# Kernel tuning notes

Hardware: AMD Instinct MI355X
Metric: run time of the kernel (lower is better)

The kernel has to match this reference:

```python
import jax, jax.numpy as jnp
import numpy as np

N_NODES = 20000
N_EDGES = 320000
N_GRAPHS = 256
F_IN = 128
HID = 512


def _xavier(key, shape, gain=1.0):
    fan_out, fan_in = shape
    a = gain * np.sqrt(6.0 / (fan_in + fan_out))
    return jax.random.uniform(key, shape, jnp.float32, -a, a)


def setup_inputs() -> dict:
    key = jax.random.key(0)
    ks = jax.random.split(key, 9)
    x = jax.random.normal(ks[0], (N_NODES, F_IN), jnp.float32)
    edge_index = jax.random.randint(ks[1], (2, N_EDGES), 0, N_NODES, dtype=jnp.int64)
    batch = jnp.sort(jax.random.randint(ks[2], (N_NODES,), 0, N_GRAPHS, dtype=jnp.int64))
    return {
        "x": x,
        "edge_index": edge_index,
        "batch": batch,
        "lin_W": _xavier(ks[3], (HID, F_IN)),
        "lin_b": jnp.zeros((HID,), jnp.float32),
        "W1": _xavier(ks[4], (HID, F_IN)),
        "b1": jnp.zeros((HID,), jnp.float32),
        "W2": _xavier(ks[5], (HID, HID)),
        "b2": jnp.zeros((HID,), jnp.float32),
        "W3": _xavier(ks[6], (HID, HID)),
        "b3": jnp.zeros((HID,), jnp.float32),
        "W4": _xavier(ks[7], (HID, HID)),
        "b4": jnp.zeros((HID,), jnp.float32),
    }


def _gcn_conv(x, W, b, src, dst, norm, n_nodes):
    # PyG GCNConv: h = x @ W.T; out_i = sum_j norm_ij * h_j (scatter over dst) + b
    h = x @ W.T
    msg = h[src] * norm[:, None]  # [E', H] gather + scale
    return jax.ops.segment_sum(msg, dst, num_segments=n_nodes) + b


def reference(x, edge_index, batch, lin_W, lin_b, W1, b1, W2, b2, W3, b3, W4, b4):
    n = x.shape[0]
    loop = jnp.arange(n, dtype=edge_index.dtype)
    src = jnp.concatenate([edge_index[0], loop])
    dst = jnp.concatenate([edge_index[1], loop])
    # symmetric normalization D^-1/2 (A+I) D^-1/2, degree = in-degree over dst
    deg = jax.ops.segment_sum(jnp.ones_like(src, dtype=x.dtype), dst, num_segments=n)
    dis = jnp.where(deg > 0, jax.lax.rsqrt(deg), 0.0)
    norm = dis[src] * dis[dst]

    x_l = x @ lin_W.T + lin_b  # dead code when act=None (kept for faithfulness)

    h1 = _gcn_conv(x, W1, b1, src, dst, norm, n)
    h2 = _gcn_conv(h1, W2, b2, src, dst, norm, n)
    h3 = _gcn_conv(h2, W3, b3, src, dst, norm, n)
    h4 = _gcn_conv(h3, W4, b4, src, dst, norm, n)
    h = jnp.concatenate([h1, h2, h3, h4], axis=1)  # [N, 4*HID]

    h_pooled = jax.ops.segment_max(h, batch, num_segments=N_GRAPHS)
    h_pos = (h > 0).astype(h.dtype)
    counts = jax.ops.segment_sum(jnp.ones((n,), h.dtype), batch, num_segments=N_GRAPHS)
    h_pos_pooled = jax.ops.segment_sum(h_pos, batch, num_segments=N_GRAPHS) / jnp.maximum(counts, 1.0)[:, None]
    return jnp.concatenate([h_pooled, h_pos_pooled], axis=1)  # [G, 8*HID]
```

## Files before the change

kernel.cpp:

```cpp
#include <hip/hip_runtime.h>
#include <cfloat>
#include <cmath>

#define F_IN 128
#define HID 512

typedef short bf16x8 __attribute__((ext_vector_type(8)));
typedef float f32x4 __attribute__((ext_vector_type(4)));
typedef short s16x4 __attribute__((ext_vector_type(4)));

__device__ static inline void split_bf16(float v, short& hi, short& lo) {
    unsigned u = __float_as_uint(v);
    unsigned r = u + 0x7FFF + ((u >> 16) & 1);
    hi = (short)(r >> 16);
    float hf = __uint_as_float(((unsigned)(unsigned short)hi) << 16);
    float res = v - hf;
    unsigned u2 = __float_as_uint(res);
    unsigned r2 = u2 + 0x7FFF + ((u2 >> 16) & 1);
    lo = (short)(r2 >> 16);
}

__device__ static inline void gload_lds16(const void* g, void* l) {
    __builtin_amdgcn_global_load_lds(
        (const __attribute__((address_space(1))) unsigned int*)g,
        (__attribute__((address_space(3))) unsigned int*)l,
        16, 0, 0);
}


__global__ void zero_kernel(int* __restrict__ a, int n) {
    int i = blockIdx.x * blockDim.x + threadIdx.x;
    if (i < n) a[i] = 0;
}

__global__ void count_in_kernel(const int* __restrict__ dst, int* __restrict__ cnt, int E) {
    int e = blockIdx.x * blockDim.x + threadIdx.x;
    if (e < E) atomicAdd(&cnt[dst[e]], 1);
}

__global__ void scan_kernel(const int* __restrict__ cnt, int* __restrict__ offs, int n) {
    __shared__ int buf[1024];
    __shared__ int carry_s;
    if (threadIdx.x == 0) carry_s = 0;
    __syncthreads();
    for (int base = 0; base < n; base += 1024) {
        int i = base + threadIdx.x;
        int v = (i < n) ? cnt[i] : 0;
        buf[threadIdx.x] = v;
        __syncthreads();
        for (int s = 1; s < 1024; s <<= 1) {
            int t = (threadIdx.x >= s) ? buf[threadIdx.x - s] : 0;
            __syncthreads();
            buf[threadIdx.x] += t;
            __syncthreads();
        }
        int total = buf[1023];
        if (i < n) offs[i] = carry_s + buf[threadIdx.x] - v;
        __syncthreads();
        if (threadIdx.x == 0) carry_s += total;
        __syncthreads();
    }
    if (threadIdx.x == 0) offs[n] = carry_s;
}

__global__ void dis_starts_kernel(const int* __restrict__ offs, float* __restrict__ dis,
                                  float* __restrict__ rdis,
                                  const int* __restrict__ batch, int* __restrict__ starts,
                                  int n, int G) {
    int i = blockIdx.x * blockDim.x + threadIdx.x;
    if (i >= n) return;
    float degp1 = (float)(offs[i + 1] - offs[i] + 1);
    dis[i] = rsqrtf(degp1);
    rdis[i] = sqrtf(degp1);
    int b = batch[i];
    if (i == 0) {
        for (int g = 0; g <= b; g++) starts[g] = 0;
    } else {
        int bp = batch[i - 1];
        for (int g = bp + 1; g <= b; g++) starts[g] = i;
    }
    if (i == n - 1) {
        for (int g = b + 1; g <= G; g++) starts[g] = n;
    }
}

__global__ void fill_csr_kernel(const int* __restrict__ src, const int* __restrict__ dst,
                                const int* __restrict__ offs, int* __restrict__ cnt,
                                unsigned short* __restrict__ csr, int E) {
    int e = blockIdx.x * blockDim.x + threadIdx.x;
    if (e < E) {
        int d = dst[e];
        int p = atomicSub(&cnt[d], 1);
        csr[offs[d] + p - 1] = (unsigned short)src[e];
    }
}

__global__ void wconv_kernel(const float* __restrict__ W1, const float* __restrict__ W2,
                             const float* __restrict__ W3, const float* __restrict__ W4,
                             short* __restrict__ Whi, short* __restrict__ Wlo) {
    int i = blockIdx.x * blockDim.x + threadIdx.x;
    const int n1 = HID * F_IN, nk = HID * HID;
    float v;
    if (i < n1) v = W1[i];
    else if (i < n1 + nk) v = W2[i - n1];
    else if (i < n1 + 2 * nk) v = W3[i - n1 - nk];
    else if (i < n1 + 3 * nk) v = W4[i - n1 - 2 * nk];
    else return;
    short h, l;
    split_bf16(v, h, l);
    Whi[i] = h;
    Wlo[i] = l;
}

__global__ void xscale_kernel(const float* __restrict__ x, const float* __restrict__ dis,
                              float* __restrict__ xs, int total) {
    int i = blockIdx.x * blockDim.x + threadIdx.x;
    if (i < total) xs[i] = x[i] * dis[i >> 7];
}

template <int F, int CHUNKS>
__global__ __launch_bounds__(256) void agg_gather4_kernel(
    const float* __restrict__ Hs, const float* __restrict__ dis,
    const int* __restrict__ offs, const unsigned short* __restrict__ csr,
    short* __restrict__ Ahi, short* __restrict__ Alo, int n) {
    constexpr int CW = 128;
    int blk = blockIdx.x;
    int chunk = blk & (CHUNKS - 1);
    int gt = blk / CHUNKS;
    int wave = threadIdx.x >> 6;
    int i = gt * 4 + wave;
    if (i >= n) return;

    int tid = threadIdx.x & 63;
    int es = tid >> 5;
    int lq = tid & 31;
    int colbase = chunk * CW + lq * 4;
    const float* Hbase = Hs + colbase;

    int e0 = offs[i], e1 = offs[i + 1];
    float di = dis[i];

    f32x4 acc = (f32x4){0.f, 0.f, 0.f, 0.f};
    if (es == 0) acc = *(const f32x4*)(Hbase + (size_t)i * F);

    for (int w0 = e0; w0 < e1; w0 += 64) {
        int cnt = e1 - w0; if (cnt > 64) cnt = 64;
        int idx = n;
        if (tid < cnt) idx = csr[w0 + tid];
        int nb4 = (cnt + 7) >> 3;
        for (int b = 0; b < nb4; b++) {
            int base = b * 8 + es;
            int j0 = __shfl(idx, base,     64);
            int j1 = __shfl(idx, base + 2, 64);
            int j2 = __shfl(idx, base + 4, 64);
            int j3 = __shfl(idx, base + 6, 64);
            f32x4 r0 = *(const f32x4*)(Hbase + (size_t)j0 * F);
            f32x4 r1 = *(const f32x4*)(Hbase + (size_t)j1 * F);
            f32x4 r2 = *(const f32x4*)(Hbase + (size_t)j2 * F);
            f32x4 r3 = *(const f32x4*)(Hbase + (size_t)j3 * F);
            acc[0] += (r0[0] + r1[0]) + (r2[0] + r3[0]);
            acc[1] += (r0[1] + r1[1]) + (r2[1] + r3[1]);
            acc[2] += (r0[2] + r1[2]) + (r2[2] + r3[2]);
            acc[3] += (r0[3] + r1[3]) + (r2[3] + r3[3]);
        }
    }
    acc[0] += __shfl_xor(acc[0], 32, 64);
    acc[1] += __shfl_xor(acc[1], 32, 64);
    acc[2] += __shfl_xor(acc[2], 32, 64);
    acc[3] += __shfl_xor(acc[3], 32, 64);

    if (es == 0) {
        short h[4], l[4];
        #pragma unroll
        for (int q = 0; q < 4; q++) split_bf16(acc[q] * di, h[q], l[q]);
        *(s16x4*)&Ahi[(size_t)i * F + colbase] = (s16x4){h[0], h[1], h[2], h[3]};
        *(s16x4*)&Alo[(size_t)i * F + colbase] = (s16x4){l[0], l[1], l[2], l[3]};
    }
}

__global__ __launch_bounds__(256) void gemm_mfma_kernel(
    const short* __restrict__ Ahi, const short* __restrict__ Alo,
    const short* __restrict__ Whi, const short* __restrict__ Wlo,
    const float* __restrict__ bias, const float* __restrict__ dis,
    float* __restrict__ Hs,
    int M, int K, int Nout, int MT, int MT8) {
    __shared__ __attribute__((aligned(16))) short lds[12288];

    int blk = blockIdx.x;
    int xcd = blk & 7;
    int r = blk >> 3;
    int n0t = r & 7;
    int mt = xcd * MT8 + (r >> 3);
    if (mt >= MT) return;
    int m0 = mt * 128, n0 = n0t * 64;

    int tid = threadIdx.x;
    int w = tid >> 6, l = tid & 63;
    int lrow = l & 15, lq = l >> 4;
    int w6 = w * 6;

    f32x4 acc[4][2];
    #pragma unroll
    for (int i = 0; i < 4; i++)
        #pragma unroll
        for (int j = 0; j < 2; j++) acc[i][j] = (f32x4){0.f, 0.f, 0.f, 0.f};

    int wm = w >> 1, wn = w & 1;

    for (int k0 = 0; k0 < K; k0 += 32) {
        #pragma unroll
        for (int t = 0; t < 6; t++) {
            int s = w6 + t;
            const short* pl;
            int prow;
            if (s < 8)       { pl = Ahi; prow = m0 + 16 * s; }
            else if (s < 16) { pl = Alo; prow = m0 + 16 * (s - 8); }
            else if (s < 20) { pl = Whi; prow = n0 + 16 * (s - 16); }
            else             { pl = Wlo; prow = n0 + 16 * (s - 20); }
            gload_lds16(pl + (size_t)(prow + lrow) * K + (k0 + lq * 8), &lds[s * 512]);
        }
        __syncthreads();

        bf16x8 ah[4], al[4], wh[2], wl[2];
        #pragma unroll
        for (int i = 0; i < 4; i++) {
            ah[i] = *(const bf16x8*)&lds[((wm * 4 + i) * 64 + l) * 8];
            al[i] = *(const bf16x8*)&lds[((8 + wm * 4 + i) * 64 + l) * 8];
        }
        #pragma unroll
        for (int j = 0; j < 2; j++) {
            wh[j] = *(const bf16x8*)&lds[((16 + wn * 2 + j) * 64 + l) * 8];
            wl[j] = *(const bf16x8*)&lds[((20 + wn * 2 + j) * 64 + l) * 8];
        }
        #pragma unroll
        for (int i = 0; i < 4; i++)
            #pragma unroll
            for (int j = 0; j < 2; j++) {
                acc[i][j] = __builtin_amdgcn_mfma_f32_16x16x32_bf16(ah[i], wh[j], acc[i][j], 0, 0, 0);
                acc[i][j] = __builtin_amdgcn_mfma_f32_16x16x32_bf16(ah[i], wl[j], acc[i][j], 0, 0, 0);
                acc[i][j] = __builtin_amdgcn_mfma_f32_16x16x32_bf16(al[i], wh[j], acc[i][j], 0, 0, 0);
            }
        __syncthreads();
    }

    float dv[4][4];
    #pragma unroll
    for (int i = 0; i < 4; i++) {
        int mrow = m0 + (wm * 4 + i) * 16 + lq * 4;
        #pragma unroll
        for (int rr = 0; rr < 4; rr++) {
            int mm = mrow + rr;
            dv[i][rr] = (mm < M) ? dis[mm] : 0.0f;
        }
    }

    #pragma unroll
    for (int j = 0; j < 2; j++) {
        int col = n0 + (wn * 2 + j) * 16 + lrow;
        float bv = bias[col];
        #pragma unroll
        for (int i = 0; i < 4; i++) {
            int mrow = m0 + (wm * 4 + i) * 16 + lq * 4;
            #pragma unroll
            for (int rr = 0; rr < 4; rr++) {
                int mm = mrow + rr;
                if (mm < M) Hs[(size_t)mm * Nout + col] = dv[i][rr] * (acc[i][j][rr] + bv);
            }
        }
    }
}

__global__ __launch_bounds__(64) void pool_kernel(
    const float* __restrict__ Hs, const float* __restrict__ rdis,
    const int* __restrict__ starts,
    float* __restrict__ out, int layer) {
    int g = blockIdx.x;
    int c = blockIdx.y * 64 + threadIdx.x;
    int s = starts[g], e = starts[g + 1];
    float mx = -INFINITY;
    int pos = 0;
    #pragma unroll 4
    for (int n = s; n < e; n++) {
        float v = Hs[(size_t)n * HID + c] * rdis[n];
        mx = fmaxf(mx, v);
        pos += (v > 0.0f) ? 1 : 0;
    }
    float cntf = fmaxf((float)(e - s), 1.0f);
    out[(size_t)g * (8 * HID) + layer * HID + c] = mx;
    out[(size_t)g * (8 * HID) + 4 * HID + layer * HID + c] = (float)pos / cntf;
}

extern "C" void kernel_launch(void* const* d_in, const int* in_sizes, int n_in,
                              void* d_out, int out_size, void* d_ws, size_t ws_size,
                              hipStream_t stream) {
    const float* x     = (const float*)d_in[0];
    const int*   eidx  = (const int*)d_in[1];
    const int*   batch = (const int*)d_in[2];
    const float* W1 = (const float*)d_in[5];
    const float* b1 = (const float*)d_in[6];
    const float* W2 = (const float*)d_in[7];
    const float* b2 = (const float*)d_in[8];
    const float* W3 = (const float*)d_in[9];
    const float* b3 = (const float*)d_in[10];
    const float* W4 = (const float*)d_in[11];
    const float* b4 = (const float*)d_in[12];
    float* out = (float*)d_out;

    const int N = in_sizes[0] / F_IN;
    const int E = in_sizes[1] / 2;
    const int G = out_size / (8 * HID);

    const int* src = eidx;
    const int* dst = eidx + E;

    const size_t nW = (size_t)HID * F_IN + 3 * (size_t)HID * HID;
    char* w = (char*)d_ws;
    short* Ahi = (short*)w; w += (size_t)N * HID * sizeof(short);
    short* Alo = (short*)w; w += (size_t)N * HID * sizeof(short);
    float* Hs  = (float*)w; w += (size_t)(N + 1) * HID * sizeof(float);
    float* xs  = (float*)w; w += (size_t)(N + 1) * F_IN * sizeof(float);
    short* Whi = (short*)w; w += nW * sizeof(short);
    short* Wlo = (short*)w; w += nW * sizeof(short);
    int* offs  = (int*)w;   w += (size_t)(N + 4) * sizeof(int);
    unsigned short* csr = (unsigned short*)w; w += (size_t)E * sizeof(unsigned short);
    int* cnt   = (int*)w;   w += (size_t)N * sizeof(int);
    float* dis = (float*)w; w += (size_t)N * sizeof(float);
    float* rdis = (float*)w; w += (size_t)N * sizeof(float);
    int* starts = (int*)w;  w += (size_t)(G + 1) * sizeof(int);

    const size_t wo1 = 0;
    const size_t wo2 = (size_t)HID * F_IN;
    const size_t wo3 = wo2 + (size_t)HID * HID;
    const size_t wo4 = wo3 + (size_t)HID * HID;

    const int TB = 256;
    zero_kernel<<<(N + TB - 1) / TB, TB, 0, stream>>>(cnt, N);
    zero_kernel<<<(HID + TB - 1) / TB, TB, 0, stream>>>((int*)(Hs + (size_t)N * HID), HID);
    zero_kernel<<<1, TB, 0, stream>>>((int*)(xs + (size_t)N * F_IN), F_IN);
    count_in_kernel<<<(E + TB - 1) / TB, TB, 0, stream>>>(dst, cnt, E);
    scan_kernel<<<1, 1024, 0, stream>>>(cnt, offs, N);
    dis_starts_kernel<<<(N + TB - 1) / TB, TB, 0, stream>>>(offs, dis, rdis, batch, starts, N, G);
    fill_csr_kernel<<<(E + TB - 1) / TB, TB, 0, stream>>>(src, dst, offs, cnt, csr, E);
    wconv_kernel<<<((int)nW + TB - 1) / TB, TB, 0, stream>>>(W1, W2, W3, W4, Whi, Wlo);
    xscale_kernel<<<(N * F_IN + TB - 1) / TB, TB, 0, stream>>>(x, dis, xs, N * F_IN);

    const int MT = (N + 127) / 128;
    const int MT8 = (MT + 7) / 8;
    const int gemm_blocks = 8 * MT8 * 8;
    dim3 pool_grid(G, HID / 64);

    const int NG = (N + 3) / 4;
    const int agg1_blocks = NG * 1;
    const int aggh_blocks = NG * 4;

    agg_gather4_kernel<F_IN, 1><<<agg1_blocks, 256, 0, stream>>>(xs, dis, offs, csr, Ahi, Alo, N);
    gemm_mfma_kernel<<<gemm_blocks, 256, 0, stream>>>(Ahi, Alo, Whi + wo1, Wlo + wo1, b1, dis, Hs,
                                                      N, F_IN, HID, MT, MT8);
    pool_kernel<<<pool_grid, 64, 0, stream>>>(Hs, rdis, starts, out, 0);

    const size_t wos[3] = {wo2, wo3, wo4};
    const float* bs_[3] = {b2, b3, b4};
    for (int ll = 0; ll < 3; ll++) {
        agg_gather4_kernel<HID, 4><<<aggh_blocks, 256, 0, stream>>>(Hs, dis, offs, csr, Ahi, Alo, N);
        gemm_mfma_kernel<<<gemm_blocks, 256, 0, stream>>>(Ahi, Alo, Whi + wos[ll], Wlo + wos[ll], bs_[ll], dis, Hs,
                                                          N, HID, HID, MT, MT8);
        pool_kernel<<<pool_grid, 64, 0, stream>>>(Hs, rdis, starts, out, ll + 1);
    }
}
```

Before: 706.0 us.

## Double-buffer LDS tiles in split-bf16 MFMA GEMM to overlap loads with compute

The GEMM kernel now keeps two LDS buffers and issues the global-to-LDS loads for the next K tile before running the MFMAs on the current one, with one barrier per iteration instead of two. Per-thread source pointers and offsets are precomputed once outside the loop. This hides global load latency behind the matrix multiply. In exchange it doubles LDS use per block, which may lower occupancy. It also depends on the manual vmcnt wait plus barrier to order the asynchronous LDS writes correctly.

```diff
diff --git a/kernel.cpp b/kernel.cpp
--- a/kernel.cpp
+++ b/kernel.cpp
@@ -184,7 +184,7 @@
     const float* __restrict__ bias, const float* __restrict__ dis,
     float* __restrict__ Hs,
     int M, int K, int Nout, int MT, int MT8) {
-    __shared__ __attribute__((aligned(16))) short lds[12288];
+    __shared__ __attribute__((aligned(16))) short lds[2][12288];
 
     int blk = blockIdx.x;
     int xcd = blk & 7;
@@ -199,6 +199,23 @@
     int lrow = l & 15, lq = l >> 4;
     int w6 = w * 6;
 
+    const short* spl[6];
+    size_t soff[6];
+    int sseg[6];
+    #pragma unroll
+    for (int t = 0; t < 6; t++) {
+        int s = w6 + t;
+        const short* pl;
+        int prow;
+        if (s < 8)       { pl = Ahi; prow = m0 + 16 * s; }
+        else if (s < 16) { pl = Alo; prow = m0 + 16 * (s - 8); }
+        else if (s < 20) { pl = Whi; prow = n0 + 16 * (s - 16); }
+        else             { pl = Wlo; prow = n0 + 16 * (s - 20); }
+        spl[t] = pl;
+        soff[t] = (size_t)(prow + lrow) * K + lq * 8;
+        sseg[t] = s * 512;
+    }
+
     f32x4 acc[4][2];
     #pragma unroll
     for (int i = 0; i < 4; i++)
@@ -207,30 +224,32 @@
 
     int wm = w >> 1, wn = w & 1;
 
-    for (int k0 = 0; k0 < K; k0 += 32) {
-        #pragma unroll
-        for (int t = 0; t < 6; t++) {
-            int s = w6 + t;
-            const short* pl;
-            int prow;
-            if (s < 8)       { pl = Ahi; prow = m0 + 16 * s; }
-            else if (s < 16) { pl = Alo; prow = m0 + 16 * (s - 8); }
-            else if (s < 20) { pl = Whi; prow = n0 + 16 * (s - 16); }
-            else             { pl = Wlo; prow = n0 + 16 * (s - 20); }
-            gload_lds16(pl + (size_t)(prow + lrow) * K + (k0 + lq * 8), &lds[s * 512]);
-        }
-        __syncthreads();
+    #pragma unroll
+    for (int t = 0; t < 6; t++)
+        gload_lds16(spl[t] + soff[t], &lds[0][sseg[t]]);
+    asm volatile("s_waitcnt vmcnt(0)" ::: "memory");
+    __builtin_amdgcn_s_barrier();
+
+    const int nt = K >> 5;
+    int cur = 0;
+    for (int t = 0; t < nt; t++) {
+        if (t + 1 < nt) {
+            size_t kadd = (size_t)(t + 1) * 32;
+            #pragma unroll
+            for (int s = 0; s < 6; s++)
+                gload_lds16(spl[s] + soff[s] + kadd, &lds[cur ^ 1][sseg[s]]);
+        }
 
         bf16x8 ah[4], al[4], wh[2], wl[2];
         #pragma unroll
         for (int i = 0; i < 4; i++) {
-            ah[i] = *(const bf16x8*)&lds[((wm * 4 + i) * 64 + l) * 8];
-            al[i] = *(const bf16x8*)&lds[((8 + wm * 4 + i) * 64 + l) * 8];
+            ah[i] = *(const bf16x8*)&lds[cur][((wm * 4 + i) * 64 + l) * 8];
+            al[i] = *(const bf16x8*)&lds[cur][((8 + wm * 4 + i) * 64 + l) * 8];
         }
         #pragma unroll
         for (int j = 0; j < 2; j++) {
-            wh[j] = *(const bf16x8*)&lds[((16 + wn * 2 + j) * 64 + l) * 8];
-            wl[j] = *(const bf16x8*)&lds[((20 + wn * 2 + j) * 64 + l) * 8];
+            wh[j] = *(const bf16x8*)&lds[cur][((16 + wn * 2 + j) * 64 + l) * 8];
+            wl[j] = *(const bf16x8*)&lds[cur][((20 + wn * 2 + j) * 64 + l) * 8];
         }
         #pragma unroll
         for (int i = 0; i < 4; i++)
@@ -240,7 +259,10 @@
                 acc[i][j] = __builtin_amdgcn_mfma_f32_16x16x32_bf16(ah[i], wl[j], acc[i][j], 0, 0, 0);
                 acc[i][j] = __builtin_amdgcn_mfma_f32_16x16x32_bf16(al[i], wh[j], acc[i][j], 0, 0, 0);
             }
-        __syncthreads();
+
+        asm volatile("s_waitcnt vmcnt(0)" ::: "memory");
+        __builtin_amdgcn_s_barrier();
+        cur ^= 1;
     }
 
     float dv[4][4];
```

After: 667.6 us. -5.4%, faster.
